# Kernel optimization log

Hardware: AMD Instinct MI355X
Metric: run time of the kernel (lower is better)

Reference implementation:

```python
import jax, jax.numpy as jnp
import numpy as np

T = 128          # number_of_trees
B = 1024         # batch_size
D = 28 * 28      # hardcoded feature dim
K = 200          # hardcoded top-k


def setup_inputs() -> dict:
    key = jax.random.key(0)
    k1, k2 = jax.random.split(key)
    x = jax.random.normal(k1, (B, D), dtype=jnp.float32)
    attention_mask = jax.random.uniform(k2, (T, D), dtype=jnp.float32, minval=-1.0, maxval=1.0)
    return {"x": x, "attention_mask": attention_mask}


def reference(x, attention_mask):
    # sigmoid -> top-k -> scatter builds a sparse per-tree mask [T, D]
    att = jax.nn.sigmoid(attention_mask)                      # [T, D]
    topk, idx = jax.lax.top_k(att, K)                         # [T, K] each
    rows = jnp.arange(T)[:, None]                             # [T, 1]
    attention = jnp.zeros((T, D), dtype=att.dtype).at[rows, idx].set(topk)  # [T, D]
    # per-tree broadcast multiply, vectorized (replaces python loop over trees)
    xf = x.reshape(-1, D)                                     # [B, D]
    return_value = xf[:, None, :] * attention[None, :, :]     # [B, T, D]
    return (return_value, attention)
```

## Files before the change

### kernel.cpp

```cpp
#include <hip/hip_runtime.h>
#include <math.h>

#define NT 128
#define NB 1024
#define ND 784
#define NK 200
#define ND4 196
#define TND4 (NT * ND4)
#define HALF4 (TND4 / 2)

typedef float vfloat4 __attribute__((ext_vector_type(4)));

__global__ __launch_bounds__(256) void topk_attention_kernel(
    const float* __restrict__ mask, float* __restrict__ att_out)
{
    __shared__ int wsum[32][4];
    __shared__ int wtie[4][4];

    const int t    = blockIdx.x;
    const int tid  = threadIdx.x;
    const int wave = tid >> 6;
    const int lane = tid & 63;

    unsigned int key[4];
    float        val[4];
    #pragma unroll
    for (int j = 0; j < 4; ++j) {
        const int d = tid + j * 256;
        if (d < ND) {
            const float f = mask[t * ND + d];
            const unsigned int b = __float_as_uint(f);
            key[j] = ((int)b < 0) ? ~b : (b | 0x80000000u);
            val[j] = 1.0f / (1.0f + expf(-f));
        } else { key[j] = 0u; val[j] = 0.0f; }
    }

    unsigned int p = 0;
    int need = NK;
    for (int bit = 31; bit >= 0; --bit) {
        const unsigned int test = (p >> bit) | 1u;
        int c = 0;
        #pragma unroll
        for (int j = 0; j < 4; ++j) c += ((key[j] >> bit) == test) ? 1 : 0;
        #pragma unroll
        for (int off = 32; off > 0; off >>= 1) c += __shfl_down(c, off);
        if (lane == 0) wsum[bit][wave] = c;
        __syncthreads();
        const int tot = wsum[bit][0] + wsum[bit][1] + wsum[bit][2] + wsum[bit][3];
        if (tot >= need) p |= (1u << bit);
        else             need -= tot;
    }

    int rankw[4];
    #pragma unroll
    for (int j = 0; j < 4; ++j) {
        const bool tie = (key[j] == p);
        const unsigned long long m = __ballot(tie);
        rankw[j] = __popcll(m & ((1ull << lane) - 1ull));
        if (lane == 0) wtie[j][wave] = __popcll(m);
    }
    __syncthreads();
    int jbase[4];
    {
        int pre = 0;
        #pragma unroll
        for (int j = 0; j < 4; ++j) {
            jbase[j] = pre;
            pre += wtie[j][0] + wtie[j][1] + wtie[j][2] + wtie[j][3];
        }
    }

    #pragma unroll
    for (int j = 0; j < 4; ++j) {
        const int d = tid + j * 256;
        if (d < ND) {
            bool keep = key[j] > p;
            if (key[j] == p) {
                int off = jbase[j] + rankw[j];
                for (int w = 0; w < 4; ++w) if (w < wave) off += wtie[j][w];
                keep = off < need;
            }
            att_out[t * ND + d] = keep ? val[j] : 0.0f;
        }
    }
}

__global__ __launch_bounds__(256) void bcast_mul_kernel(
    const vfloat4* __restrict__ x4, const vfloat4* __restrict__ att4,
    vfloat4* __restrict__ out4)
{
    const int b = blockIdx.y;
    const int k = blockIdx.x * 256 + threadIdx.x;
    const unsigned int t = (unsigned int)k / 196u;
    const int d4 = k - (int)(t * 196u);

    const vfloat4 xs = x4[b * ND4 + d4];
    const vfloat4 a0 = att4[k];
    const vfloat4 a1 = att4[k + HALF4];

    vfloat4* __restrict__ ob = out4 + (size_t)b * TND4 + k;
    ob[0]     = a0 * xs;
    ob[HALF4] = a1 * xs;
}

extern "C" void kernel_launch(void* const* d_in, const int* in_sizes, int n_in,
                              void* d_out, int out_size, void* d_ws, size_t ws_size,
                              hipStream_t stream)
{
    (void)in_sizes; (void)n_in; (void)out_size; (void)d_ws; (void)ws_size;
    const float* x    = (const float*)d_in[0];
    const float* mask = (const float*)d_in[1];
    float* out = (float*)d_out;
    float* att = out + (size_t)NB * NT * ND;

    topk_attention_kernel<<<NT, 256, 0, stream>>>(mask, att);
    bcast_mul_kernel<<<dim3(HALF4 / 256, NB), 256, 0, stream>>>(
        (const vfloat4*)x, (const vfloat4*)att, (vfloat4*)out);
}
```

Measured before the change: 436.1 us.

## Use grid-stride broadcast multiply with prefetch and nontemporal stores

Replaces the 2D grid of one-block-per-batch-row with a fixed 1024-block grid-stride loop over the whole output. Each iteration prefetches the next att/x values before storing the current product. Stores use nontemporal hints so the 411MB output stream does not pollute cache. The catch is more integer div/mod per element and a fixed grid size that may underfill or oversubscribe the CUs.

```diff
diff --git a/kernel.cpp b/kernel.cpp
--- a/kernel.cpp
+++ b/kernel.cpp
@@ -7,7 +7,9 @@
 #define NK 200
 #define ND4 196
 #define TND4 (NT * ND4)
-#define HALF4 (TND4 / 2)
+#define TOTAL4 (NB * TND4)
+#define GTHREADS (1024 * 256)
+#define ITERS (TOTAL4 / GTHREADS)
 
 typedef float vfloat4 __attribute__((ext_vector_type(4)));
 
@@ -89,18 +91,26 @@
     const vfloat4* __restrict__ x4, const vfloat4* __restrict__ att4,
     vfloat4* __restrict__ out4)
 {
-    const int b = blockIdx.y;
-    const int k = blockIdx.x * 256 + threadIdx.x;
-    const unsigned int t = (unsigned int)k / 196u;
-    const int d4 = k - (int)(t * 196u);
+    unsigned n = blockIdx.x * 256u + threadIdx.x;
 
-    const vfloat4 xs = x4[b * ND4 + d4];
-    const vfloat4 a0 = att4[k];
-    const vfloat4 a1 = att4[k + HALF4];
+    unsigned b  = n / (unsigned)TND4;
+    unsigned r  = n - b * (unsigned)TND4;
+    unsigned d4 = r % (unsigned)ND4;
+    vfloat4 a  = att4[r];
+    vfloat4 xs = x4[b * (unsigned)ND4 + d4];
 
-    vfloat4* __restrict__ ob = out4 + (size_t)b * TND4 + k;
-    ob[0]     = a0 * xs;
-    ob[HALF4] = a1 * xs;
+    #pragma unroll 2
+    for (int it = 0; it < ITERS - 1; ++it) {
+        const unsigned n2  = n + (unsigned)GTHREADS;
+        const unsigned b2  = n2 / (unsigned)TND4;
+        const unsigned r2  = n2 - b2 * (unsigned)TND4;
+        const unsigned d42 = r2 % (unsigned)ND4;
+        const vfloat4 a2  = att4[r2];
+        const vfloat4 x2  = x4[b2 * (unsigned)ND4 + d42];
+        __builtin_nontemporal_store(a * xs, &out4[n]);
+        n = n2; a = a2; xs = x2;
+    }
+    __builtin_nontemporal_store(a * xs, &out4[n]);
 }
 
 extern "C" void kernel_launch(void* const* d_in, const int* in_sizes, int n_in,
@@ -114,6 +124,6 @@
     float* att = out + (size_t)NB * NT * ND;
 
     topk_attention_kernel<<<NT, 256, 0, stream>>>(mask, att);
-    bcast_mul_kernel<<<dim3(HALF4 / 256, NB), 256, 0, stream>>>(
+    bcast_mul_kernel<<<GTHREADS / 256, 256, 0, stream>>>(
         (const vfloat4*)x, (const vfloat4*)att, (vfloat4*)out);
 }
```

Measured after the change: 448.8 us. 2.9% more time.
